# Kernel optimization log

Hardware: AMD Instinct MI355X
Metric: run time of the kernel (lower is better)

Reference implementation:

```python
import jax, jax.numpy as jnp
import numpy as np

ALPHA = 0.2          # leaky_relu negative slope
NEG_INF = -9e15      # mask fill value (matches torch source)


def setup_inputs() -> dict:
    key = jax.random.key(0)
    k_h, k_mask, k_W, k_a = jax.random.split(key, 4)
    B, N, F_in, F_out = 4, 65536, 128, 128
    h = jax.random.normal(k_h, (B, N, F_in), dtype=jnp.float32)
    # op_mask > 0 means "mask out this neighbor" (prev/self/next)
    op_mask = jax.random.randint(k_mask, (B, N, 3), 0, 2, dtype=jnp.int32)
    # xavier_uniform-style init for params
    lim_W = 1.414 * np.sqrt(6.0 / (F_in + F_out))
    W = jax.random.uniform(k_W, (F_in, F_out), dtype=jnp.float32, minval=-lim_W, maxval=lim_W)
    lim_a = 1.414 * np.sqrt(6.0 / (2 * F_out + 1))
    a = jax.random.uniform(k_a, (2 * F_out, 1), dtype=jnp.float32, minval=-lim_a, maxval=lim_a)
    return {"h": h, "op_mask": op_mask, "W": W, "a": a}


def reference(h, op_mask, W, a):
    F_out = W.shape[1]
    Wh = jnp.matmul(h, W)                                   # [B, N, F]
    # windowed neighbors: prev (roll +1), self, next (roll -1)
    Wh_concat = jnp.stack(
        [jnp.roll(Wh, 1, axis=1), Wh, jnp.roll(Wh, -1, axis=1)], axis=-2
    )                                                       # [B, N, 3, F]
    Wh1 = jnp.matmul(Wh, a[:F_out])                         # [B, N, 1]
    Wh2 = jnp.matmul(Wh, a[F_out:])                         # [B, N, 1]
    Wh2_concat = jnp.stack(
        [jnp.roll(Wh2, 1, axis=1), Wh2, jnp.roll(Wh2, -1, axis=1)], axis=-1
    )                                                       # [B, N, 1, 3]
    e = jax.nn.leaky_relu(Wh1[..., None] + Wh2_concat, ALPHA)  # [B, N, 1, 3]
    e = jnp.where(op_mask[:, :, None, :] > 0, jnp.float32(NEG_INF), e)
    attention = jax.nn.softmax(e, axis=-1)                  # [B, N, 1, 3]
    # dropout_prob = 0.0 (eval-equivalent), so dropout is identity
    h_new = jnp.matmul(attention, Wh_concat).squeeze(-2)    # [B, N, F]
    return h_new
```

## Files before the change

### kernel.cpp

```cpp
#include <hip/hip_runtime.h>
#include <hip/hip_bf16.h>

typedef __attribute__((ext_vector_type(8))) short short8;
typedef __attribute__((ext_vector_type(4))) float f32x4;

#define ALPHA 0.2f
#define NEG_INF -9e15f
#define OUT_ROWS 126
#define NTILES 521
#define NB 4
#define NN 65536

typedef __attribute__((address_space(3))) void as3_void;
typedef const __attribute__((address_space(1))) void as1_void;

__device__ __forceinline__ short fb(float x) {
    __hip_bfloat16 b = __float2bfloat16(x);
    return __builtin_bit_cast(short, b);
}

__global__ __launch_bounds__(256) void prep_w(const float* __restrict__ W,
                                              const float* __restrict__ a,
                                              unsigned short* __restrict__ ws) {
    const int t = threadIdx.x;
    if (blockIdx.x < 8) {
        int q = blockIdx.x * 256 + t;
        int lane = q & 63, fi = q >> 6;
        int ni = fi & 3, kk = (fi >> 2) & 3, wcg = fi >> 4;
        int n = wcg * 64 + ni * 16 + (lane & 15);
        int k0 = kk * 32 + ((lane >> 4) & 3) * 8;
        short8 o;
        #pragma unroll
        for (int j = 0; j < 8; ++j) o[j] = fb(W[(k0 + j) * 128 + n]);
        *(short8*)(ws + (size_t)q * 8) = o;
    } else {
        __shared__ float wa[2][128];
        {
            int k = t >> 1, sel = t & 1;
            const f32x4* wr4 = (const f32x4*)(W + k * 128);
            const f32x4* av4 = (const f32x4*)(a + sel * 128);
            float s = 0.f;
            #pragma unroll
            for (int c4 = 0; c4 < 32; ++c4) {
                f32x4 wv = wr4[c4], av = av4[c4];
                s += wv[0]*av[0] + wv[1]*av[1] + wv[2]*av[2] + wv[3]*av[3];
            }
            wa[sel][k] = s;
        }
        __syncthreads();
        {
            int lane = t & 63, kk = t >> 6;
            int l15 = lane & 15, lg = (lane >> 4) & 3;
            int k0 = kk * 32 + lg * 8;
            short8 o;
            #pragma unroll
            for (int j = 0; j < 8; ++j) {
                float v = (l15 < 2) ? wa[l15][k0 + j] : 0.f;
                o[j] = fb(v);
            }
            *(short8*)(ws + 16384 + (size_t)t * 8) = o;
        }
    }
}

__global__ __launch_bounds__(256, 2)
void gat_fused(const float* __restrict__ h, const int* __restrict__ opm,
               const unsigned short* __restrict__ ws, float* __restrict__ out) {
    __shared__ __align__(16) char smem[65536];
    __shared__ float wh1_s[128];
    __shared__ float wh2_s[128];
    __shared__ float att_s[128][4];

    const int t = threadIdx.x;
    int orig = blockIdx.x;
    int xcd = orig & 7, idx = orig >> 3;
    int wgid = (xcd < 4 ? xcd * 261 : 1044 + (xcd - 4) * 260) + idx;
    const int b = wgid / NTILES;
    const int tile = wgid - b * NTILES;
    const int row_start = tile * OUT_ROWS;
    const int out_rows = min(OUT_ROWS, NN - row_start);
    const float* hB = h + (size_t)b * NN * 128;
    float* outB = out + (size_t)b * NN * 128;

    const int lane = t & 63;
    const int wave = t >> 6;

    int m0 = 0, m1 = 0, m2 = 0;
    if (t >= 1 && t <= out_rows) {
        const int* mr = opm + ((size_t)b * NN + row_start + t - 1) * 3;
        m0 = mr[0]; m1 = mr[1]; m2 = mr[2];
    }

    {
        const char* hC = (const char*)hB;
        #pragma unroll
        for (int i = 0; i < 16; ++i) {
            int rpair = (wave << 4) + i;
            int r = (rpair << 1) + (lane >> 5);
            int g = row_start - 1 + r;
            if (g < 0) g += NN;
            if (g >= NN) g -= NN;
            const char* src = hC + (size_t)g * 512 +
                              (((lane & 31) << 4) ^ ((r & 7) << 4));
            char* dst = smem + (rpair << 10);
            __builtin_amdgcn_global_load_lds((as1_void*)src, (as3_void*)dst, 16, 0, 0);
        }
    }
    __syncthreads();

    const int l15 = lane & 15;
    const int lg = (lane >> 4) & 3;
    const int wr = (wave >> 1) << 6;
    const int wcg = wave & 1;
    const int wc = wcg << 6;

    f32x4 acc[4][4];
    f32x4 acc2[4];
    #pragma unroll
    for (int mi = 0; mi < 4; ++mi) {
        acc2[mi] = (f32x4){0.f, 0.f, 0.f, 0.f};
        #pragma unroll
        for (int ni = 0; ni < 4; ++ni)
            acc[mi][ni] = (f32x4){0.f, 0.f, 0.f, 0.f};
    }

    const short8* wsv  = (const short8*)ws;
    const short8* wsv2 = (const short8*)(ws + 16384);
    #pragma unroll
    for (int kk = 0; kk < 4; ++kk) {
        short8 bfr[4], bfr2;
        #pragma unroll
        for (int ni = 0; ni < 4; ++ni)
            bfr[ni] = wsv[((((wcg << 2) + kk) << 2) + ni) * 64 + lane];
        bfr2 = wsv2[(kk << 6) + lane];
        int kb = (kk << 7) + (lg << 5);
        short8 af[4];
        #pragma unroll
        for (int mi = 0; mi < 4; ++mi) {
            int m = wr + (mi << 4) + l15;
            int sw = (m & 7) << 4;
            const char* base = smem + m * 512;
            f32x4 lo = *(const f32x4*)(base + (kb ^ sw));
            f32x4 hi = *(const f32x4*)(base + ((kb + 16) ^ sw));
            short8 v;
            v[0] = fb(lo[0]); v[1] = fb(lo[1]); v[2] = fb(lo[2]); v[3] = fb(lo[3]);
            v[4] = fb(hi[0]); v[5] = fb(hi[1]); v[6] = fb(hi[2]); v[7] = fb(hi[3]);
            af[mi] = v;
        }
        #pragma unroll
        for (int mi = 0; mi < 4; ++mi) {
            #pragma unroll
            for (int ni = 0; ni < 4; ++ni)
                acc[mi][ni] = __builtin_amdgcn_mfma_f32_16x16x32_bf16(
                    af[mi], bfr[ni], acc[mi][ni], 0, 0, 0);
            acc2[mi] = __builtin_amdgcn_mfma_f32_16x16x32_bf16(
                af[mi], bfr2, acc2[mi], 0, 0, 0);
        }
    }
    __syncthreads();

    #pragma unroll
    for (int mi = 0; mi < 4; ++mi)
        #pragma unroll
        for (int ni = 0; ni < 4; ++ni) {
            int col = wc + (ni << 4) + l15;
            #pragma unroll
            for (int j = 0; j < 4; ++j) {
                int row = wr + (mi << 4) + (lg << 2) + j;
                *(float*)(smem + row * 512 + ((col << 2) ^ ((row & 7) << 4))) =
                    acc[mi][ni][j];
            }
        }
    if (l15 < 2) {
        float* dv = (l15 == 0) ? wh1_s : wh2_s;
        #pragma unroll
        for (int mi = 0; mi < 4; ++mi)
            #pragma unroll
            for (int j = 0; j < 4; ++j)
                dv[wr + (mi << 4) + (lg << 2) + j] = acc2[mi][j];
    }
    __syncthreads();

    if (t >= 1 && t <= out_rows) {
        float w1 = wh1_s[t];
        float e0 = w1 + wh2_s[t - 1];
        float e1 = w1 + wh2_s[t];
        float e2 = w1 + wh2_s[t + 1];
        e0 = e0 > 0.f ? e0 : ALPHA * e0;
        e1 = e1 > 0.f ? e1 : ALPHA * e1;
        e2 = e2 > 0.f ? e2 : ALPHA * e2;
        if (m0 > 0) e0 = NEG_INF;
        if (m1 > 0) e1 = NEG_INF;
        if (m2 > 0) e2 = NEG_INF;
        float m = fmaxf(e0, fmaxf(e1, e2));
        float x0 = __expf(e0 - m), x1 = __expf(e1 - m), x2 = __expf(e2 - m);
        float inv = 1.f / (x0 + x1 + x2);
        att_s[t][0] = x0 * inv;
        att_s[t][1] = x1 * inv;
        att_s[t][2] = x2 * inv;
    }
    __syncthreads();

    #pragma unroll
    for (int it = 0; it < 16; ++it) {
        int rr = 1 + (t >> 5) + (it << 3);
        if (rr > out_rows) continue;
        int cb = (t & 31) << 4;
        float a0 = att_s[rr][0], a1 = att_s[rr][1], a2 = att_s[rr][2];
        f32x4 wm = *(const f32x4*)(smem + (rr - 1) * 512 + (cb ^ (((rr - 1) & 7) << 4)));
        f32x4 w0 = *(const f32x4*)(smem + rr * 512 + (cb ^ ((rr & 7) << 4)));
        f32x4 wp = *(const f32x4*)(smem + (rr + 1) * 512 + (cb ^ (((rr + 1) & 7) << 4)));
        f32x4 res;
        #pragma unroll
        for (int j = 0; j < 4; ++j)
            res[j] = a0 * wm[j] + a1 * w0[j] + a2 * wp[j];
        float* op = outB + (size_t)(row_start + rr - 1) * 128 + ((t & 31) << 2);
        __builtin_nontemporal_store(res, (f32x4*)op);
    }
}

extern "C" void kernel_launch(void* const* d_in, const int* in_sizes, int n_in,
                              void* d_out, int out_size, void* d_ws, size_t ws_size,
                              hipStream_t stream) {
    const float* h   = (const float*)d_in[0];
    const int*   opm = (const int*)d_in[1];
    const float* W   = (const float*)d_in[2];
    const float* a   = (const float*)d_in[3];
    float* out = (float*)d_out;
    unsigned short* ws = (unsigned short*)d_ws;
    prep_w<<<9, 256, 0, stream>>>(W, a, ws);
    gat_fused<<<NTILES * NB, 256, 0, stream>>>(h, opm, ws, out);
}
```

Before: 64.62 us.

## Persistent double-buffered GAT kernel with register prefetch and in-register neighbor mixing

Converts the one-tile-per-block kernel into a persistent kernel with 512 blocks that loop over tiles. Each block prefetches the next tile's h rows into registers, converts them to bf16 and stores them into a double-buffered LDS. The weight fragments are held in registers for the whole kernel. The attention-weighted neighbor combination now reads the rows above and below from the MFMA accumulators through lane shuffles plus small boundary arrays, so the fp32 Wh tile no longer goes back to LDS. The cost is much higher register pressure and scalar, uncoalesced 4-byte output stores in place of 16-byte nontemporal stores. The mask loads also move into the epilogue.

```diff
diff --git a/kernel.cpp b/kernel.cpp
--- a/kernel.cpp
+++ b/kernel.cpp
@@ -10,9 +10,8 @@
 #define NTILES 521
 #define NB 4
 #define NN 65536
-
-typedef __attribute__((address_space(3))) void as3_void;
-typedef const __attribute__((address_space(1))) void as1_void;
+#define TOT (NTILES * NB)
+#define GRID 512
 
 __device__ __forceinline__ short fb(float x) {
     __hip_bfloat16 b = __float2bfloat16(x);
@@ -54,10 +53,7 @@
             int k0 = kk * 32 + lg * 8;
             short8 o;
             #pragma unroll
-            for (int j = 0; j < 8; ++j) {
-                float v = (l15 < 2) ? wa[l15][k0 + j] : 0.f;
-                o[j] = fb(v);
-            }
+            for (int j = 0; j < 8; ++j) o[j] = fb((l15 < 2) ? wa[l15][k0 + j] : 0.f);
             *(short8*)(ws + 16384 + (size_t)t * 8) = o;
         }
     }
@@ -66,156 +62,222 @@
 __global__ __launch_bounds__(256, 2)
 void gat_fused(const float* __restrict__ h, const int* __restrict__ opm,
                const unsigned short* __restrict__ ws, float* __restrict__ out) {
-    __shared__ __align__(16) char smem[65536];
-    __shared__ float wh1_s[128];
-    __shared__ float wh2_s[128];
-    __shared__ float att_s[128][4];
+    __shared__ __align__(16) char bufs[2][32768];
+    __shared__ float wh1s[2][128];
+    __shared__ float wh2s[2][136];
+    __shared__ float bds[2][2][128];
 
     const int t = threadIdx.x;
-    int orig = blockIdx.x;
-    int xcd = orig & 7, idx = orig >> 3;
-    int wgid = (xcd < 4 ? xcd * 261 : 1044 + (xcd - 4) * 260) + idx;
-    const int b = wgid / NTILES;
-    const int tile = wgid - b * NTILES;
-    const int row_start = tile * OUT_ROWS;
-    const int out_rows = min(OUT_ROWS, NN - row_start);
-    const float* hB = h + (size_t)b * NN * 128;
-    float* outB = out + (size_t)b * NN * 128;
-
     const int lane = t & 63;
     const int wave = t >> 6;
-
-    int m0 = 0, m1 = 0, m2 = 0;
-    if (t >= 1 && t <= out_rows) {
-        const int* mr = opm + ((size_t)b * NN + row_start + t - 1) * 3;
-        m0 = mr[0]; m1 = mr[1]; m2 = mr[2];
-    }
-
-    {
-        const char* hC = (const char*)hB;
-        #pragma unroll
-        for (int i = 0; i < 16; ++i) {
-            int rpair = (wave << 4) + i;
-            int r = (rpair << 1) + (lane >> 5);
-            int g = row_start - 1 + r;
-            if (g < 0) g += NN;
-            if (g >= NN) g -= NN;
-            const char* src = hC + (size_t)g * 512 +
-                              (((lane & 31) << 4) ^ ((r & 7) << 4));
-            char* dst = smem + (rpair << 10);
-            __builtin_amdgcn_global_load_lds((as1_void*)src, (as3_void*)dst, 16, 0, 0);
-        }
-    }
-    __syncthreads();
-
     const int l15 = lane & 15;
     const int lg = (lane >> 4) & 3;
     const int wr = (wave >> 1) << 6;
     const int wcg = wave & 1;
     const int wc = wcg << 6;
 
-    f32x4 acc[4][4];
-    f32x4 acc2[4];
-    #pragma unroll
-    for (int mi = 0; mi < 4; ++mi) {
-        acc2[mi] = (f32x4){0.f, 0.f, 0.f, 0.f};
-        #pragma unroll
-        for (int ni = 0; ni < 4; ++ni)
-            acc[mi][ni] = (f32x4){0.f, 0.f, 0.f, 0.f};
-    }
-
-    const short8* wsv  = (const short8*)ws;
-    const short8* wsv2 = (const short8*)(ws + 16384);
-    #pragma unroll
-    for (int kk = 0; kk < 4; ++kk) {
-        short8 bfr[4], bfr2;
-        #pragma unroll
-        for (int ni = 0; ni < 4; ++ni)
-            bfr[ni] = wsv[((((wcg << 2) + kk) << 2) + ni) * 64 + lane];
-        bfr2 = wsv2[(kk << 6) + lane];
-        int kb = (kk << 7) + (lg << 5);
-        short8 af[4];
+    short8 bfr[4][4];
+    short8 bfr2[4];
+    {
+        const short8* wsv  = (const short8*)ws;
+        const short8* wsv2 = (const short8*)(ws + 16384);
+        #pragma unroll
+        for (int kk = 0; kk < 4; ++kk) {
+            #pragma unroll
+            for (int ni = 0; ni < 4; ++ni)
+                bfr[kk][ni] = wsv[((((wcg << 2) + kk) << 2) + ni) * 64 + lane];
+            bfr2[kk] = wsv2[(kk << 6) + lane];
+        }
+    }
+
+    int ti = blockIdx.x;
+
+    {
+        int b = ti / NTILES;
+        int tile = ti - b * NTILES;
+        int base = tile * OUT_ROWS - 1;
+        const float* hB = h + (size_t)b * NN * 128;
+        f32x4 sreg[16];
+        #pragma unroll
+        for (int i = 0; i < 16; ++i) {
+            int rl = (wave << 5) + (i << 1) + (lane >> 5);
+            int g = base + rl;
+            if (g < 0) g += NN; else if (g >= NN) g -= NN;
+            sreg[i] = *(const f32x4*)(hB + (size_t)g * 128 + ((lane & 31) << 2));
+        }
+        #pragma unroll
+        for (int i = 0; i < 16; ++i) {
+            int rl = (wave << 5) + (i << 1) + (lane >> 5);
+            ushort4 p4;
+            p4.x = (unsigned short)fb(sreg[i][0]);
+            p4.y = (unsigned short)fb(sreg[i][1]);
+            p4.z = (unsigned short)fb(sreg[i][2]);
+            p4.w = (unsigned short)fb(sreg[i][3]);
+            *(ushort4*)(&bufs[0][rl * 256 + ((((lane & 31) << 3)) ^ ((rl & 7) << 4))]) = p4;
+        }
+    }
+    __syncthreads();
+
+    int cur = 0;
+    for (; ti < TOT; ti += GRID) {
+        const int b = ti / NTILES;
+        const int tile = ti - b * NTILES;
+        const int row_start = tile * OUT_ROWS;
+        const int base = row_start - 1;
+        const int out_rows = min(OUT_ROWS, NN - row_start);
+        float* outB = out + (size_t)b * NN * 128;
+        const int* opmB = opm + (size_t)b * NN * 3;
+
+        const int tn = ti + GRID;
+        const bool has_next = tn < TOT;
+        f32x4 sreg[16];
+        if (has_next) {
+            int b2 = tn / NTILES;
+            int tile2 = tn - b2 * NTILES;
+            int base2 = tile2 * OUT_ROWS - 1;
+            const float* hB2 = h + (size_t)b2 * NN * 128;
+            #pragma unroll
+            for (int i = 0; i < 16; ++i) {
+                int rl = (wave << 5) + (i << 1) + (lane >> 5);
+                int g = base2 + rl;
+                if (g < 0) g += NN; else if (g >= NN) g -= NN;
+                sreg[i] = *(const f32x4*)(hB2 + (size_t)g * 128 + ((lane & 31) << 2));
+            }
+        }
+
+        f32x4 acc[4][4];
+        f32x4 acc2[4];
         #pragma unroll
         for (int mi = 0; mi < 4; ++mi) {
-            int m = wr + (mi << 4) + l15;
-            int sw = (m & 7) << 4;
-            const char* base = smem + m * 512;
-            f32x4 lo = *(const f32x4*)(base + (kb ^ sw));
-            f32x4 hi = *(const f32x4*)(base + ((kb + 16) ^ sw));
-            short8 v;
-            v[0] = fb(lo[0]); v[1] = fb(lo[1]); v[2] = fb(lo[2]); v[3] = fb(lo[3]);
-            v[4] = fb(hi[0]); v[5] = fb(hi[1]); v[6] = fb(hi[2]); v[7] = fb(hi[3]);
-            af[mi] = v;
-        }
+            acc2[mi] = (f32x4){0.f, 0.f, 0.f, 0.f};
+            #pragma unroll
+            for (int ni = 0; ni < 4; ++ni)
+                acc[mi][ni] = (f32x4){0.f, 0.f, 0.f, 0.f};
+        }
+        #pragma unroll
+        for (int kk = 0; kk < 4; ++kk) {
+            int kb = (kk << 6) + (lg << 4);
+            short8 af[4];
+            #pragma unroll
+            for (int mi = 0; mi < 4; ++mi) {
+                int m = wr + (mi << 4) + l15;
+                af[mi] = *(const short8*)(&bufs[cur][m * 256 + (kb ^ ((m & 7) << 4))]);
+            }
+            #pragma unroll
+            for (int mi = 0; mi < 4; ++mi)
+                #pragma unroll
+                for (int ni = 0; ni < 4; ++ni)
+                    acc[mi][ni] = __builtin_amdgcn_mfma_f32_16x16x32_bf16(
+                        af[mi], bfr[kk][ni], acc[mi][ni], 0, 0, 0);
+            if (wcg == 0) {
+                #pragma unroll
+                for (int mi = 0; mi < 4; ++mi)
+                    acc2[mi] = __builtin_amdgcn_mfma_f32_16x16x32_bf16(
+                        af[mi], bfr2[kk], acc2[mi], 0, 0, 0);
+            }
+        }
+
+        const int p = cur;
+        if (wcg == 0 && l15 < 2) {
+            float* dst = (l15 == 0) ? wh1s[p] : (wh2s[p] + 4);
+            #pragma unroll
+            for (int mi = 0; mi < 4; ++mi)
+                #pragma unroll
+                for (int j = 0; j < 4; ++j)
+                    dst[wr + (mi << 4) + (lg << 2) + j] = acc2[mi][j];
+        }
+        if (wr == 0) {
+            if (lg == 3) {
+                #pragma unroll
+                for (int ni = 0; ni < 4; ++ni)
+                    bds[p][0][wc + (ni << 4) + l15] = acc[3][ni][3];
+            }
+        } else {
+            if (lg == 0) {
+                #pragma unroll
+                for (int ni = 0; ni < 4; ++ni)
+                    bds[p][1][wc + (ni << 4) + l15] = acc[0][ni][0];
+            }
+        }
+
+        if (has_next) {
+            #pragma unroll
+            for (int i = 0; i < 16; ++i) {
+                int rl = (wave << 5) + (i << 1) + (lane >> 5);
+                ushort4 p4;
+                p4.x = (unsigned short)fb(sreg[i][0]);
+                p4.y = (unsigned short)fb(sreg[i][1]);
+                p4.z = (unsigned short)fb(sreg[i][2]);
+                p4.w = (unsigned short)fb(sreg[i][3]);
+                *(ushort4*)(&bufs[cur ^ 1][rl * 256 + ((((lane & 31) << 3)) ^ ((rl & 7) << 4))]) = p4;
+            }
+        }
+        __syncthreads();
+
+        float S[4][4], P[4][4];
+        const int ln_n = (lane + 16) & 63;
+        const int ln_p = (lane + 48) & 63;
+        #pragma unroll
+        for (int mi = 0; mi < 4; ++mi)
+            #pragma unroll
+            for (int ni = 0; ni < 4; ++ni) {
+                S[mi][ni] = __shfl(acc[mi][ni][0], ln_n);
+                P[mi][ni] = __shfl(acc[mi][ni][3], ln_p);
+            }
+        float bd0v[4], bd1v[4];
+        #pragma unroll
+        for (int ni = 0; ni < 4; ++ni) {
+            bd0v[ni] = bds[p][0][wc + (ni << 4) + l15];
+            bd1v[ni] = bds[p][1][wc + (ni << 4) + l15];
+        }
+
         #pragma unroll
         for (int mi = 0; mi < 4; ++mi) {
-            #pragma unroll
-            for (int ni = 0; ni < 4; ++ni)
-                acc[mi][ni] = __builtin_amdgcn_mfma_f32_16x16x32_bf16(
-                    af[mi], bfr[ni], acc[mi][ni], 0, 0, 0);
-            acc2[mi] = __builtin_amdgcn_mfma_f32_16x16x32_bf16(
-                af[mi], bfr2, acc2[mi], 0, 0, 0);
-        }
-    }
-    __syncthreads();
-
-    #pragma unroll
-    for (int mi = 0; mi < 4; ++mi)
-        #pragma unroll
-        for (int ni = 0; ni < 4; ++ni) {
-            int col = wc + (ni << 4) + l15;
+            int r0 = wr + (mi << 4) + (lg << 2);
+            f32x4 w1v = *(const f32x4*)(wh1s[p] + r0);
+            f32x4 w2a = *(const f32x4*)(wh2s[p] + r0);
+            f32x4 w2b = *(const f32x4*)(wh2s[p] + 4 + r0);
+            f32x4 w2c = *(const f32x4*)(wh2s[p] + 8 + r0);
+            float av[4][3];
             #pragma unroll
             for (int j = 0; j < 4; ++j) {
-                int row = wr + (mi << 4) + (lg << 2) + j;
-                *(float*)(smem + row * 512 + ((col << 2) ^ ((row & 7) << 4))) =
-                    acc[mi][ni][j];
-            }
-        }
-    if (l15 < 2) {
-        float* dv = (l15 == 0) ? wh1_s : wh2_s;
-        #pragma unroll
-        for (int mi = 0; mi < 4; ++mi)
-            #pragma unroll
-            for (int j = 0; j < 4; ++j)
-                dv[wr + (mi << 4) + (lg << 2) + j] = acc2[mi][j];
-    }
-    __syncthreads();
-
-    if (t >= 1 && t <= out_rows) {
-        float w1 = wh1_s[t];
-        float e0 = w1 + wh2_s[t - 1];
-        float e1 = w1 + wh2_s[t];
-        float e2 = w1 + wh2_s[t + 1];
-        e0 = e0 > 0.f ? e0 : ALPHA * e0;
-        e1 = e1 > 0.f ? e1 : ALPHA * e1;
-        e2 = e2 > 0.f ? e2 : ALPHA * e2;
-        if (m0 > 0) e0 = NEG_INF;
-        if (m1 > 0) e1 = NEG_INF;
-        if (m2 > 0) e2 = NEG_INF;
-        float m = fmaxf(e0, fmaxf(e1, e2));
-        float x0 = __expf(e0 - m), x1 = __expf(e1 - m), x2 = __expf(e2 - m);
-        float inv = 1.f / (x0 + x1 + x2);
-        att_s[t][0] = x0 * inv;
-        att_s[t][1] = x1 * inv;
-        att_s[t][2] = x2 * inv;
-    }
-    __syncthreads();
-
-    #pragma unroll
-    for (int it = 0; it < 16; ++it) {
-        int rr = 1 + (t >> 5) + (it << 3);
-        if (rr > out_rows) continue;
-        int cb = (t & 31) << 4;
-        float a0 = att_s[rr][0], a1 = att_s[rr][1], a2 = att_s[rr][2];
-        f32x4 wm = *(const f32x4*)(smem + (rr - 1) * 512 + (cb ^ (((rr - 1) & 7) << 4)));
-        f32x4 w0 = *(const f32x4*)(smem + rr * 512 + (cb ^ ((rr & 7) << 4)));
-        f32x4 wp = *(const f32x4*)(smem + (rr + 1) * 512 + (cb ^ (((rr + 1) & 7) << 4)));
-        f32x4 res;
-        #pragma unroll
-        for (int j = 0; j < 4; ++j)
-            res[j] = a0 * wm[j] + a1 * w0[j] + a2 * wp[j];
-        float* op = outB + (size_t)(row_start + rr - 1) * 128 + ((t & 31) << 2);
-        __builtin_nontemporal_store(res, (f32x4*)op);
+                int r = r0 + j;
+                int g = base + r;
+                int gc = g < 0 ? 0 : (g >= NN ? NN - 1 : g);
+                const int* mrow = opmB + (size_t)gc * 3;
+                int mk0 = mrow[0], mk1 = mrow[1], mk2 = mrow[2];
+                float wprev = (j == 0) ? w2a[3] : w2b[j - 1];
+                float wnext = (j == 3) ? w2c[0] : w2b[j + 1];
+                float w1 = w1v[j];
+                float e0 = w1 + wprev, e1 = w1 + w2b[j], e2 = w1 + wnext;
+                e0 = e0 > 0.f ? e0 : ALPHA * e0;
+                e1 = e1 > 0.f ? e1 : ALPHA * e1;
+                e2 = e2 > 0.f ? e2 : ALPHA * e2;
+                if (mk0 > 0) e0 = NEG_INF;
+                if (mk1 > 0) e1 = NEG_INF;
+                if (mk2 > 0) e2 = NEG_INF;
+                float m = fmaxf(e0, fmaxf(e1, e2));
+                float x0 = __expf(e0 - m), x1 = __expf(e1 - m), x2 = __expf(e2 - m);
+                float inv = 1.f / (x0 + x1 + x2);
+                av[j][0] = x0 * inv; av[j][1] = x1 * inv; av[j][2] = x2 * inv;
+            }
+            #pragma unroll
+            for (int ni = 0; ni < 4; ++ni) {
+                float pv0 = (lg > 0) ? P[mi][ni] : ((mi > 0) ? P[mi - 1][ni] : bd0v[ni]);
+                float nx3 = (lg < 3) ? S[mi][ni] : ((mi < 3) ? S[mi + 1][ni] : bd1v[ni]);
+                int col = wc + (ni << 4) + l15;
+                #pragma unroll
+                for (int j = 0; j < 4; ++j) {
+                    int r = r0 + j;
+                    float pv = (j == 0) ? pv0 : acc[mi][ni][j - 1];
+                    float nx = (j == 3) ? nx3 : acc[mi][ni][j + 1];
+                    float o = av[j][0] * pv + av[j][1] * acc[mi][ni][j] + av[j][2] * nx;
+                    if (r >= 1 && r <= out_rows)
+                        outB[(size_t)(base + r) * 128 + col] = o;
+                }
+            }
+        }
+        cur ^= 1;
     }
 }
 
@@ -229,5 +291,5 @@
     float* out = (float*)d_out;
     unsigned short* ws = (unsigned short*)d_ws;
     prep_w<<<9, 256, 0, stream>>>(W, a, ws);
-    gat_fused<<<NTILES * NB, 256, 0, stream>>>(h, opm, ws, out);
-}
+    gat_fused<<<GRID, 256, 0, stream>>>(h, opm, ws, out);
+}
```

Measured after the change: 133.5 us. +106.6%, slower.
